# Performance work log

Hardware: AMD Instinct MI355X
Metric: run time of the kernel (lower is better)

## Reference

```python
import jax, jax.numpy as jnp
import numpy as np

N_NODES = 100000
N_EDGES = 800000
N_GRAPHS = 64
D_IN = 128
D_H = 256
D_MID = 64
D_OUT = 3


def _sage_conv(x, src, dst, Wl, bl, Wr, n_nodes):
    # PyG SAGEConv (mean aggr): out = lin_l(mean_{j in N(i)} x_j) + lin_r(x_i)
    msg_sum = jax.ops.segment_sum(x[src], dst, num_segments=n_nodes)   # [N, d]
    deg = jax.ops.segment_sum(jnp.ones((src.shape[0],), x.dtype), dst,
                              num_segments=n_nodes)                     # [N]
    mean = msg_sum / jnp.maximum(deg, 1.0)[:, None]
    return mean @ Wl + bl + x @ Wr


def setup_inputs() -> dict:
    key = jax.random.key(0)
    ks = jax.random.split(key, 16)
    s = 0.05
    inp = {
        "x": jax.random.normal(ks[0], (N_NODES, D_IN), dtype=jnp.float32),
        "edge_index": jax.random.randint(ks[1], (2, N_EDGES), 0, N_NODES, dtype=jnp.int32),
        "batch": jnp.sort(jax.random.randint(ks[2], (N_NODES,), 0, N_GRAPHS, dtype=jnp.int32)),
        # conv1
        "W1l": jax.random.normal(ks[3], (D_IN, D_H), dtype=jnp.float32) * s,
        "b1l": jnp.zeros((D_H,), jnp.float32),
        "W1r": jax.random.normal(ks[4], (D_IN, D_H), dtype=jnp.float32) * s,
        # conv2
        "W2l": jax.random.normal(ks[5], (D_H, D_H), dtype=jnp.float32) * s,
        "b2l": jnp.zeros((D_H,), jnp.float32),
        "W2r": jax.random.normal(ks[6], (D_H, D_H), dtype=jnp.float32) * s,
        # conv3
        "W3l": jax.random.normal(ks[7], (D_H, D_H), dtype=jnp.float32) * s,
        "b3l": jnp.zeros((D_H,), jnp.float32),
        "W3r": jax.random.normal(ks[8], (D_H, D_H), dtype=jnp.float32) * s,
        # head
        "Wlin1": jax.random.normal(ks[9], (D_H, D_MID), dtype=jnp.float32) * s,
        "blin1": jnp.zeros((D_MID,), jnp.float32),
        "Wlin2": jax.random.normal(ks[10], (D_MID, D_OUT), dtype=jnp.float32) * s,
        "blin2": jnp.zeros((D_OUT,), jnp.float32),
    }
    return inp


def reference(x, edge_index, batch, W1l, b1l, W1r, W2l, b2l, W2r,
              W3l, b3l, W3r, Wlin1, blin1, Wlin2, blin2):
    src, dst = edge_index[0], edge_index[1]
    h = jnp.tanh(_sage_conv(x, src, dst, W1l, b1l, W1r, N_NODES))
    h = jnp.tanh(_sage_conv(h, src, dst, W2l, b2l, W2r, N_NODES))
    h = _sage_conv(h, src, dst, W3l, b3l, W3r, N_NODES)
    pooled = jax.ops.segment_max(h, batch, num_segments=N_GRAPHS)  # [G, 256]
    pooled = jnp.where(jnp.isneginf(pooled), 0.0, pooled)  # empty segments -> 0
    # dropout_rate = 0.0 -> identity
    h = jnp.tanh(pooled @ Wlin1 + blin1)
    return h @ Wlin2 + blin2
```

## Files before the change

kernel.cpp:

```cpp
#include <hip/hip_runtime.h>

#define N_NODES 100000
#define N_PAD   100224
#define N_EDGES 800000
#define N_GRAPHS 64
#define D_IN 128
#define D_H 256

typedef __attribute__((ext_vector_type(8))) short bf16x8;
typedef __attribute__((ext_vector_type(8))) unsigned short u16x8;
typedef __attribute__((ext_vector_type(4))) float f32x4;

__device__ inline float bf2f(unsigned short u) {
    union { unsigned u32; float f; } x;
    x.u32 = ((unsigned)u) << 16;
    return x.f;
}
__device__ inline unsigned short f2bf(float f) {
    unsigned u = __float_as_uint(f);
    if ((u & 0x7fffffffu) > 0x7f800000u) return (unsigned short)0x7fc0;
    unsigned r = ((u >> 16) & 1u) + 0x7fffu;
    return (unsigned short)((u + r) >> 16);
}

__device__ inline unsigned enc_f32(float f) {
    unsigned u = __float_as_uint(f);
    return (u & 0x80000000u) ? ~u : (u | 0x80000000u);
}
__device__ inline float dec_f32(unsigned u) {
    unsigned v = (u & 0x80000000u) ? (u & 0x7FFFFFFFu) : ~u;
    return __uint_as_float(v);
}
#define ENC_NEG_INF 0x007FFFFFu

#define GLOAD_LDS16(g, l)                                                     \
    __builtin_amdgcn_global_load_lds(                                         \
        (const __attribute__((address_space(1))) unsigned int*)(g),           \
        (__attribute__((address_space(3))) unsigned int*)(l), 16, 0, 0)

__global__ void k_init_counts(int* __restrict__ counts) {
    int i = blockIdx.x * blockDim.x + threadIdx.x;
    if (i < N_NODES) counts[i] = 0;
}

__global__ void k_count(const int* __restrict__ dst, int* __restrict__ counts) {
    int e = blockIdx.x * blockDim.x + threadIdx.x;
    if (e < N_EDGES) atomicAdd(&counts[dst[e]], 1);
}

__global__ void k_scan_block(const int* __restrict__ counts, int* __restrict__ excl,
                             int* __restrict__ bsums) {
    __shared__ int sh[1024];
    int tid = threadIdx.x;
    int i = blockIdx.x * 1024 + tid;
    int v = (i < N_NODES) ? counts[i] : 0;
    sh[tid] = v;
    __syncthreads();
    for (int off = 1; off < 1024; off <<= 1) {
        int t = (tid >= off) ? sh[tid - off] : 0;
        __syncthreads();
        sh[tid] += t;
        __syncthreads();
    }
    if (i < N_NODES) excl[i] = sh[tid] - v;
    if (tid == 1023) bsums[blockIdx.x] = sh[1023];
}

__global__ void k_scan_top(int* __restrict__ bsums, int nb) {
    __shared__ int sh[128];
    int tid = threadIdx.x;
    int v = (tid < nb) ? bsums[tid] : 0;
    sh[tid] = v;
    __syncthreads();
    for (int off = 1; off < 128; off <<= 1) {
        int t = (tid >= off) ? sh[tid - off] : 0;
        __syncthreads();
        sh[tid] += t;
        __syncthreads();
    }
    if (tid < nb) bsums[tid] = sh[tid] - v;
}

__global__ void k_scan_finish(const int* __restrict__ excl, const int* __restrict__ bsums,
                              const int* __restrict__ counts, int* __restrict__ indptr,
                              int* __restrict__ cursor, float* __restrict__ deg_inv) {
    int i = blockIdx.x * blockDim.x + threadIdx.x;
    if (i < N_NODES) {
        int p = excl[i] + bsums[i >> 10];
        indptr[i] = p;
        cursor[i] = p;
        deg_inv[i] = 1.0f / fmaxf((float)counts[i], 1.0f);
        if (i == 0) indptr[N_NODES] = N_EDGES;
    }
}

__global__ void k_fill(const int* __restrict__ src, const int* __restrict__ dst,
                       int* __restrict__ cursor, int* __restrict__ eidx) {
    int e = blockIdx.x * blockDim.x + threadIdx.x;
    if (e < N_EDGES) {
        int pos = atomicAdd(&cursor[dst[e]], 1);
        eidx[pos] = src[e];
    }
}

__global__ void k_x2bf(const float* __restrict__ x, unsigned short* __restrict__ hx) {
    const int total = N_NODES * D_IN / 4;
    for (int i = blockIdx.x * blockDim.x + threadIdx.x; i < total;
         i += gridDim.x * blockDim.x) {
        float4 v = reinterpret_cast<const float4*>(x)[i];
        ushort4 o;
        o.x = f2bf(v.x); o.y = f2bf(v.y); o.z = f2bf(v.z); o.w = f2bf(v.w);
        reinterpret_cast<ushort4*>(hx)[i] = o;
    }
}

template <int K>
__global__ void k_wt(const float* __restrict__ W, unsigned short* __restrict__ Wt) {
    int idx = blockIdx.x * blockDim.x + threadIdx.x;
    if (idx < K * 256) {
        int k = idx >> 8, n = idx & 255;
        Wt[n * K + k] = f2bf(W[idx]);
    }
}

template <bool IN_F32>
__global__ void k_agg(const void* __restrict__ hin, const int* __restrict__ indptr,
                      const int* __restrict__ eidx, const float* __restrict__ deg_inv,
                      unsigned short* __restrict__ mean) {
    constexpr int D = IN_F32 ? 128 : 256;
    constexpr int C = IN_F32 ? 4 : 8;
    int wid = (blockIdx.x * blockDim.x + threadIdx.x) >> 6;
    int lane = threadIdx.x & 63;
    int nw = (gridDim.x * blockDim.x) >> 6;
    int half = lane >> 5;
    int l = lane & 31;
    for (int node = wid; node < N_NODES; node += nw) {
        int beg = indptr[node], end = indptr[node + 1];
        float acc[C] = {};
        for (int e = beg + half; e < end; e += 2) {
            int s = eidx[e];
            if (IN_F32) {
                float4 v = reinterpret_cast<const float4*>((const float*)hin + (size_t)s * D)[l];
                acc[0] += v.x; acc[1] += v.y; acc[2] += v.z; acc[3] += v.w;
            } else {
                u16x8 v = reinterpret_cast<const u16x8*>((const unsigned short*)hin + (size_t)s * D)[l];
#pragma unroll
                for (int j = 0; j < 8; ++j) acc[j] += bf2f((unsigned short)v[j]);
            }
        }
#pragma unroll
        for (int i = 0; i < C; ++i) acc[i] += __shfl_xor(acc[i], 32);
        if (lane < 32) {
            float inv = deg_inv[node];
            unsigned short* orow = mean + (size_t)node * D;
            if (IN_F32) {
                ushort4 o;
                o.x = f2bf(acc[0] * inv); o.y = f2bf(acc[1] * inv);
                o.z = f2bf(acc[2] * inv); o.w = f2bf(acc[3] * inv);
                reinterpret_cast<ushort4*>(orow)[l] = o;
            } else {
                u16x8 o;
#pragma unroll
                for (int j = 0; j < 8; ++j) o[j] = f2bf(acc[j] * inv);
                reinterpret_cast<u16x8*>(orow)[l] = o;
            }
        }
    }
}

template <int K, bool TANH, bool POOL>
__global__ __launch_bounds__(512)
void k_xform(const unsigned short* __restrict__ A0, const unsigned short* __restrict__ A1,
             const unsigned short* __restrict__ Bt0, const unsigned short* __restrict__ Bt1,
             const float* __restrict__ bias,
             unsigned short* __restrict__ out,
             const int* __restrict__ batch, unsigned* __restrict__ pooled) {
    __shared__ unsigned short Al[128 * 32];
    __shared__ unsigned short Bl[256 * 32];

    const int tid = threadIdx.x;
    const int lane = tid & 63;
    const int wid = tid >> 6;
    const int wr = wid >> 2;
    const int wc = wid & 3;
    const int m0 = blockIdx.x * 128;

    f32x4 acc[4][4] = {};

    const int lrow = lane >> 2;
    const int lk8 = (lane & 3) * 8;

#pragma unroll
    for (int slab = 0; slab < 2; ++slab) {
        const unsigned short* As = slab ? A1 : A0;
        const unsigned short* Bs = slab ? Bt1 : Bt0;
        for (int k0 = 0; k0 < K; k0 += 32) {
            __syncthreads();
            GLOAD_LDS16(As + (size_t)(m0 + wid * 16 + lrow) * K + k0 + lk8, &Al[wid * 512]);
#pragma unroll
            for (int cc = 0; cc < 2; ++cc) {
                int c = wid * 2 + cc;
                GLOAD_LDS16(Bs + (size_t)(c * 16 + lrow) * K + k0 + lk8, &Bl[c * 512]);
            }
            asm volatile("s_waitcnt vmcnt(0)" ::: "memory");
            __syncthreads();

            bf16x8 af[4], bfr[4];
#pragma unroll
            for (int f = 0; f < 4; ++f) {
                af[f] = *reinterpret_cast<const bf16x8*>(
                    &Al[(wr * 64 + f * 16 + (lane & 15)) * 32 + (lane >> 4) * 8]);
                bfr[f] = *reinterpret_cast<const bf16x8*>(
                    &Bl[(wc * 64 + f * 16 + (lane & 15)) * 32 + (lane >> 4) * 8]);
            }
#pragma unroll
            for (int fi = 0; fi < 4; ++fi)
#pragma unroll
                for (int fj = 0; fj < 4; ++fj)
                    acc[fi][fj] = __builtin_amdgcn_mfma_f32_16x16x32_bf16(
                        af[fi], bfr[fj], acc[fi][fj], 0, 0, 0);
        }
    }

    const int rbase = m0 + wr * 64 + (lane >> 4) * 4;
    const int cbase = wc * 64 + (lane & 15);
    if (POOL) {
#pragma unroll
        for (int fj = 0; fj < 4; ++fj) {
            int col = cbase + fj * 16;
            float bcol = bias[col];
            int curg = -1;
            float curmax = 0.f;
#pragma unroll
            for (int fi = 0; fi < 4; ++fi) {
#pragma unroll
                for (int r = 0; r < 4; ++r) {
                    int row = rbase + fi * 16 + r;
                    if (row >= N_NODES) continue;
                    float v = acc[fi][fj][r] + bcol;
                    if (TANH) v = tanhf(v);
                    int g = batch[row];
                    if (g != curg) {
                        if (curg >= 0) atomicMax(&pooled[curg * 256 + col], enc_f32(curmax));
                        curg = g;
                        curmax = v;
                    } else {
                        curmax = fmaxf(curmax, v);
                    }
                }
            }
            if (curg >= 0) atomicMax(&pooled[curg * 256 + col], enc_f32(curmax));
        }
    } else {
#pragma unroll
        for (int fi = 0; fi < 4; ++fi) {
#pragma unroll
            for (int fj = 0; fj < 4; ++fj) {
                int col = cbase + fj * 16;
                float bcol = bias[col];
#pragma unroll
                for (int r = 0; r < 4; ++r) {
                    int row = rbase + fi * 16 + r;
                    if (row >= N_NODES) continue;
                    float v = acc[fi][fj][r] + bcol;
                    if (TANH) v = tanhf(v);
                    out[(size_t)row * 256 + col] = f2bf(v);
                }
            }
        }
    }
}

__global__ void k_pool_init(unsigned* __restrict__ pooled) {
    int i = blockIdx.x * blockDim.x + threadIdx.x;
    if (i < N_GRAPHS * 256) pooled[i] = ENC_NEG_INF;
}

__global__ void k_head(const unsigned* __restrict__ pooled,
                       const float* __restrict__ W1, const float* __restrict__ b1,
                       const float* __restrict__ W2, const float* __restrict__ b2,
                       float* __restrict__ out) {
    __shared__ float p[256];
    __shared__ float hm[64];
    int g = blockIdx.x;
    int t = threadIdx.x;
    for (int k = t; k < 256; k += 64) {
        unsigned u = pooled[g * 256 + k];
        p[k] = (u == ENC_NEG_INF) ? 0.0f : dec_f32(u);
    }
    __syncthreads();
    float a = b1[t];
    for (int k = 0; k < 256; ++k) a += p[k] * W1[k * 64 + t];
    hm[t] = tanhf(a);
    __syncthreads();
    if (t < 3) {
        float o = b2[t];
        for (int m = 0; m < 64; ++m) o += hm[m] * W2[m * 3 + t];
        out[g * 3 + t] = o;
    }
}

extern "C" void kernel_launch(void* const* d_in, const int* in_sizes, int n_in,
                              void* d_out, int out_size, void* d_ws, size_t ws_size,
                              hipStream_t stream) {
    const float* x     = (const float*)d_in[0];
    const int*   ei    = (const int*)d_in[1];
    const int*   src   = ei;
    const int*   dst   = ei + N_EDGES;
    const int*   batch = (const int*)d_in[2];
    const float* W1l = (const float*)d_in[3];
    const float* b1l = (const float*)d_in[4];
    const float* W1r = (const float*)d_in[5];
    const float* W2l = (const float*)d_in[6];
    const float* b2l = (const float*)d_in[7];
    const float* W2r = (const float*)d_in[8];
    const float* W3l = (const float*)d_in[9];
    const float* b3l = (const float*)d_in[10];
    const float* W3r = (const float*)d_in[11];
    const float* Wlin1 = (const float*)d_in[12];
    const float* blin1 = (const float*)d_in[13];
    const float* Wlin2 = (const float*)d_in[14];
    const float* blin2 = (const float*)d_in[15];
    float* out = (float*)d_out;

    char* base = (char*)d_ws;
    size_t off = 0;
    auto alloc = [&](size_t bytes) { char* p = base + off; off += (bytes + 255) & ~(size_t)255; return (void*)p; };
    int*   counts  = (int*)alloc(N_NODES * 4);
    int*   indptr  = (int*)alloc((N_NODES + 1) * 4);
    int*   cursor  = (int*)alloc(N_NODES * 4);
    int*   excl    = (int*)alloc(N_NODES * 4);
    int*   bsums   = (int*)alloc(128 * 4);
    float* deg_inv = (float*)alloc(N_NODES * 4);
    unsigned* pooled = (unsigned*)alloc(N_GRAPHS * 256 * 4);
    int*   eidx    = (int*)alloc(N_EDGES * 4);
    unsigned short* Wt1l = (unsigned short*)alloc(256 * 128 * 2);
    unsigned short* Wt1r = (unsigned short*)alloc(256 * 128 * 2);
    unsigned short* Wt2l = (unsigned short*)alloc(256 * 256 * 2);
    unsigned short* Wt2r = (unsigned short*)alloc(256 * 256 * 2);
    unsigned short* Wt3l = (unsigned short*)alloc(256 * 256 * 2);
    unsigned short* Wt3r = (unsigned short*)alloc(256 * 256 * 2);
    unsigned short* M   = (unsigned short*)alloc((size_t)N_PAD * 256 * 2);
    unsigned short* hA  = (unsigned short*)alloc((size_t)N_PAD * 256 * 2);
    unsigned short* hxB = (unsigned short*)alloc((size_t)N_PAD * 256 * 2);
    unsigned short* hx = hxB;
    unsigned short* hB = hxB;

    const int NB_SCAN = (N_NODES + 1023) / 1024;

    k_init_counts<<<(N_NODES + 255) / 256, 256, 0, stream>>>(counts);
    k_count<<<(N_EDGES + 255) / 256, 256, 0, stream>>>(dst, counts);
    k_scan_block<<<NB_SCAN, 1024, 0, stream>>>(counts, excl, bsums);
    k_scan_top<<<1, 128, 0, stream>>>(bsums, NB_SCAN);
    k_scan_finish<<<(N_NODES + 255) / 256, 256, 0, stream>>>(excl, bsums, counts, indptr, cursor, deg_inv);
    k_fill<<<(N_EDGES + 255) / 256, 256, 0, stream>>>(src, dst, cursor, eidx);

    k_x2bf<<<2048, 256, 0, stream>>>(x, hx);
    k_wt<128><<<(128 * 256 + 255) / 256, 256, 0, stream>>>(W1l, Wt1l);
    k_wt<128><<<(128 * 256 + 255) / 256, 256, 0, stream>>>(W1r, Wt1r);
    k_wt<256><<<(256 * 256 + 255) / 256, 256, 0, stream>>>(W2l, Wt2l);
    k_wt<256><<<(256 * 256 + 255) / 256, 256, 0, stream>>>(W2r, Wt2r);
    k_wt<256><<<(256 * 256 + 255) / 256, 256, 0, stream>>>(W3l, Wt3l);
    k_wt<256><<<(256 * 256 + 255) / 256, 256, 0, stream>>>(W3r, Wt3r);
    k_pool_init<<<(N_GRAPHS * 256 + 255) / 256, 256, 0, stream>>>(pooled);

    dim3 ggrid(782);

    k_agg<true><<<2048, 256, 0, stream>>>(x, indptr, eidx, deg_inv, M);
    k_xform<128, true, false><<<ggrid, 512, 0, stream>>>(M, hx, Wt1l, Wt1r, b1l, hA, nullptr, nullptr);

    k_agg<false><<<2048, 256, 0, stream>>>(hA, indptr, eidx, deg_inv, M);
    k_xform<256, true, false><<<ggrid, 512, 0, stream>>>(M, hA, Wt2l, Wt2r, b2l, hB, nullptr, nullptr);

    k_agg<false><<<2048, 256, 0, stream>>>(hB, indptr, eidx, deg_inv, M);
    k_xform<256, false, true><<<ggrid, 512, 0, stream>>>(M, hB, Wt3l, Wt3r, b3l, nullptr, batch, pooled);

    k_head<<<N_GRAPHS, 64, 0, stream>>>(pooled, Wlin1, blin1, Wlin2, blin2, out);
}
```

Before: 540.9 us.

## Fuse weight transposes and pool init, widen gather edges, swizzle GEMM LDS

Merges the six weight-transpose launches into one grid-stride kernel and folds the pooled-buffer initialisation into the scan-finish kernel, which removes several small launches. The aggregation kernel now splits each wave into four 16-lane groups that each take an edge, so four neighbour rows are in flight per wave instead of two, with an extra shuffle stage for the reduction. The GEMM applies an XOR swizzle to the LDS chunk placement to reduce bank conflicts on fragment reads. Together these target launch overhead, gather latency and LDS conflicts, at the cost of more registers per aggregation lane.

```diff
diff --git a/kernel.cpp b/kernel.cpp
--- a/kernel.cpp
+++ b/kernel.cpp
@@ -83,8 +83,10 @@
 
 __global__ void k_scan_finish(const int* __restrict__ excl, const int* __restrict__ bsums,
                               const int* __restrict__ counts, int* __restrict__ indptr,
-                              int* __restrict__ cursor, float* __restrict__ deg_inv) {
+                              int* __restrict__ cursor, float* __restrict__ deg_inv,
+                              unsigned* __restrict__ pooled) {
     int i = blockIdx.x * blockDim.x + threadIdx.x;
+    if (i < N_GRAPHS * 256) pooled[i] = ENC_NEG_INF;
     if (i < N_NODES) {
         int p = excl[i] + bsums[i >> 10];
         indptr[i] = p;
@@ -114,12 +116,25 @@
     }
 }
 
-template <int K>
-__global__ void k_wt(const float* __restrict__ W, unsigned short* __restrict__ Wt) {
-    int idx = blockIdx.x * blockDim.x + threadIdx.x;
-    if (idx < K * 256) {
-        int k = idx >> 8, n = idx & 255;
-        Wt[n * K + k] = f2bf(W[idx]);
+__global__ void k_wt_all(const float* __restrict__ W1l, const float* __restrict__ W1r,
+                         const float* __restrict__ W2l, const float* __restrict__ W2r,
+                         const float* __restrict__ W3l, const float* __restrict__ W3r,
+                         unsigned short* __restrict__ T1l, unsigned short* __restrict__ T1r,
+                         unsigned short* __restrict__ T2l, unsigned short* __restrict__ T2r,
+                         unsigned short* __restrict__ T3l, unsigned short* __restrict__ T3r) {
+    const int S1 = 128 * 256, S2 = 256 * 256;
+    const int total = 2 * S1 + 4 * S2;
+    for (int idx = blockIdx.x * blockDim.x + threadIdx.x; idx < total;
+         idx += gridDim.x * blockDim.x) {
+        const float* W; unsigned short* T; int i, K;
+        if (idx < S1)           { W = W1l; T = T1l; i = idx;            K = 128; }
+        else if (idx < 2 * S1)  { W = W1r; T = T1r; i = idx - S1;       K = 128; }
+        else if (idx < 2*S1+S2) { W = W2l; T = T2l; i = idx - 2*S1;     K = 256; }
+        else if (idx < 2*S1+2*S2) { W = W2r; T = T2r; i = idx-2*S1-S2;  K = 256; }
+        else if (idx < 2*S1+3*S2) { W = W3l; T = T3l; i = idx-2*S1-2*S2; K = 256; }
+        else                    { W = W3r; T = T3r; i = idx-2*S1-3*S2;  K = 256; }
+        int k = i >> 8, n = i & 255;
+        T[n * K + k] = f2bf(W[(size_t)k * 256 + n]);
     }
 }
 
@@ -128,41 +143,52 @@
                       const int* __restrict__ eidx, const float* __restrict__ deg_inv,
                       unsigned short* __restrict__ mean) {
     constexpr int D = IN_F32 ? 128 : 256;
-    constexpr int C = IN_F32 ? 4 : 8;
+    constexpr int CA = IN_F32 ? 8 : 16;
     int wid = (blockIdx.x * blockDim.x + threadIdx.x) >> 6;
     int lane = threadIdx.x & 63;
     int nw = (gridDim.x * blockDim.x) >> 6;
-    int half = lane >> 5;
-    int l = lane & 31;
+    int g = lane >> 4;
+    int l16 = lane & 15;
     for (int node = wid; node < N_NODES; node += nw) {
         int beg = indptr[node], end = indptr[node + 1];
-        float acc[C] = {};
-        for (int e = beg + half; e < end; e += 2) {
+        float acc[CA] = {};
+        for (int e = beg + g; e < end; e += 4) {
             int s = eidx[e];
             if (IN_F32) {
-                float4 v = reinterpret_cast<const float4*>((const float*)hin + (size_t)s * D)[l];
-                acc[0] += v.x; acc[1] += v.y; acc[2] += v.z; acc[3] += v.w;
+                const float4* row = reinterpret_cast<const float4*>((const float*)hin + (size_t)s * D);
+                float4 v0 = row[l16 * 2], v1 = row[l16 * 2 + 1];
+                acc[0] += v0.x; acc[1] += v0.y; acc[2] += v0.z; acc[3] += v0.w;
+                acc[4] += v1.x; acc[5] += v1.y; acc[6] += v1.z; acc[7] += v1.w;
             } else {
-                u16x8 v = reinterpret_cast<const u16x8*>((const unsigned short*)hin + (size_t)s * D)[l];
-#pragma unroll
-                for (int j = 0; j < 8; ++j) acc[j] += bf2f((unsigned short)v[j]);
-            }
-        }
-#pragma unroll
-        for (int i = 0; i < C; ++i) acc[i] += __shfl_xor(acc[i], 32);
-        if (lane < 32) {
+                const u16x8* row = reinterpret_cast<const u16x8*>((const unsigned short*)hin + (size_t)s * D);
+                u16x8 v0 = row[l16 * 2], v1 = row[l16 * 2 + 1];
+#pragma unroll
+                for (int j = 0; j < 8; ++j) acc[j] += bf2f((unsigned short)v0[j]);
+#pragma unroll
+                for (int j = 0; j < 8; ++j) acc[8 + j] += bf2f((unsigned short)v1[j]);
+            }
+        }
+#pragma unroll
+        for (int i = 0; i < CA; ++i) {
+            acc[i] += __shfl_xor(acc[i], 16);
+            acc[i] += __shfl_xor(acc[i], 32);
+        }
+        if (g == 0) {
             float inv = deg_inv[node];
-            unsigned short* orow = mean + (size_t)node * D;
+            unsigned short* orow = mean + (size_t)node * (IN_F32 ? 128 : 256);
             if (IN_F32) {
-                ushort4 o;
-                o.x = f2bf(acc[0] * inv); o.y = f2bf(acc[1] * inv);
-                o.z = f2bf(acc[2] * inv); o.w = f2bf(acc[3] * inv);
-                reinterpret_cast<ushort4*>(orow)[l] = o;
+                u16x8 o;
+#pragma unroll
+                for (int j = 0; j < 8; ++j) o[j] = f2bf(acc[j] * inv);
+                reinterpret_cast<u16x8*>(orow)[l16] = o;
             } else {
-                u16x8 o;
-#pragma unroll
-                for (int j = 0; j < 8; ++j) o[j] = f2bf(acc[j] * inv);
-                reinterpret_cast<u16x8*>(orow)[l] = o;
+                u16x8 o0, o1;
+#pragma unroll
+                for (int j = 0; j < 8; ++j) o0[j] = f2bf(acc[j] * inv);
+#pragma unroll
+                for (int j = 0; j < 8; ++j) o1[j] = f2bf(acc[8 + j] * inv);
+                reinterpret_cast<u16x8*>(orow)[l16 * 2] = o0;
+                reinterpret_cast<u16x8*>(orow)[l16 * 2 + 1] = o1;
             }
         }
     }
@@ -181,14 +207,15 @@
     const int tid = threadIdx.x;
     const int lane = tid & 63;
     const int wid = tid >> 6;
-    const int wr = wid >> 2;
+    const int wr = wid >> 1 >> 1;
     const int wc = wid & 3;
     const int m0 = blockIdx.x * 128;
 
+    const int srow = lane >> 2;
+    const int schunk = (lane & 3) ^ ((lane >> 3) & 3);
+    const int koffs = schunk * 8;
+
     f32x4 acc[4][4] = {};
-
-    const int lrow = lane >> 2;
-    const int lk8 = (lane & 3) * 8;
 
 #pragma unroll
     for (int slab = 0; slab < 2; ++slab) {
@@ -196,11 +223,13 @@
         const unsigned short* Bs = slab ? Bt1 : Bt0;
         for (int k0 = 0; k0 < K; k0 += 32) {
             __syncthreads();
-            GLOAD_LDS16(As + (size_t)(m0 + wid * 16 + lrow) * K + k0 + lk8, &Al[wid * 512]);
+            GLOAD_LDS16(As + (size_t)(m0 + wid * 16 + srow) * K + k0 + koffs,
+                        &Al[wid * 512]);
 #pragma unroll
             for (int cc = 0; cc < 2; ++cc) {
                 int c = wid * 2 + cc;
-                GLOAD_LDS16(Bs + (size_t)(c * 16 + lrow) * K + k0 + lk8, &Bl[c * 512]);
+                GLOAD_LDS16(Bs + (size_t)(c * 16 + srow) * K + k0 + koffs,
+                            &Bl[c * 512]);
             }
             asm volatile("s_waitcnt vmcnt(0)" ::: "memory");
             __syncthreads();
@@ -208,10 +237,12 @@
             bf16x8 af[4], bfr[4];
 #pragma unroll
             for (int f = 0; f < 4; ++f) {
-                af[f] = *reinterpret_cast<const bf16x8*>(
-                    &Al[(wr * 64 + f * 16 + (lane & 15)) * 32 + (lane >> 4) * 8]);
-                bfr[f] = *reinterpret_cast<const bf16x8*>(
-                    &Bl[(wc * 64 + f * 16 + (lane & 15)) * 32 + (lane >> 4) * 8]);
+                int ra = wr * 64 + f * 16 + (lane & 15);
+                int pa = ((lane >> 4) ^ ((ra >> 1) & 3)) * 8;
+                af[f] = *reinterpret_cast<const bf16x8*>(&Al[ra * 32 + pa]);
+                int rb = wc * 64 + f * 16 + (lane & 15);
+                int pb = ((lane >> 4) ^ ((rb >> 1) & 3)) * 8;
+                bfr[f] = *reinterpret_cast<const bf16x8*>(&Bl[rb * 32 + pb]);
             }
 #pragma unroll
             for (int fi = 0; fi < 4; ++fi)
@@ -269,11 +300,6 @@
             }
         }
     }
-}
-
-__global__ void k_pool_init(unsigned* __restrict__ pooled) {
-    int i = blockIdx.x * blockDim.x + threadIdx.x;
-    if (i < N_GRAPHS * 256) pooled[i] = ENC_NEG_INF;
 }
 
 __global__ void k_head(const unsigned* __restrict__ pooled,
@@ -352,17 +378,12 @@
     k_count<<<(N_EDGES + 255) / 256, 256, 0, stream>>>(dst, counts);
     k_scan_block<<<NB_SCAN, 1024, 0, stream>>>(counts, excl, bsums);
     k_scan_top<<<1, 128, 0, stream>>>(bsums, NB_SCAN);
-    k_scan_finish<<<(N_NODES + 255) / 256, 256, 0, stream>>>(excl, bsums, counts, indptr, cursor, deg_inv);
+    k_scan_finish<<<(N_NODES + 255) / 256, 256, 0, stream>>>(excl, bsums, counts, indptr, cursor, deg_inv, pooled);
     k_fill<<<(N_EDGES + 255) / 256, 256, 0, stream>>>(src, dst, cursor, eidx);
 
     k_x2bf<<<2048, 256, 0, stream>>>(x, hx);
-    k_wt<128><<<(128 * 256 + 255) / 256, 256, 0, stream>>>(W1l, Wt1l);
-    k_wt<128><<<(128 * 256 + 255) / 256, 256, 0, stream>>>(W1r, Wt1r);
-    k_wt<256><<<(256 * 256 + 255) / 256, 256, 0, stream>>>(W2l, Wt2l);
-    k_wt<256><<<(256 * 256 + 255) / 256, 256, 0, stream>>>(W2r, Wt2r);
-    k_wt<256><<<(256 * 256 + 255) / 256, 256, 0, stream>>>(W3l, Wt3l);
-    k_wt<256><<<(256 * 256 + 255) / 256, 256, 0, stream>>>(W3r, Wt3r);
-    k_pool_init<<<(N_GRAPHS * 256 + 255) / 256, 256, 0, stream>>>(pooled);
+    k_wt_all<<<1280, 256, 0, stream>>>(W1l, W1r, W2l, W2r, W3l, W3r,
+                                       Wt1l, Wt1r, Wt2l, Wt2r, Wt3l, Wt3r);
 
     dim3 ggrid(782);
 
```

Result: faster. 514.8 us (-4.8%).
